# Optimization experiments

Hardware: AMD Instinct MI355X
Metric: run time of the kernel (lower is better)

Reference implementation:

```python
import jax, jax.numpy as jnp
import numpy as np

SQRT2 = 1.4142135623730951

def _gelu(x):
    return x * 0.5 * (1.0 + jax.lax.erf(x / SQRT2))

def _layer_norm(x, w, b, eps=1e-12):
    u = x.mean(-1, keepdims=True)
    s = ((x - u) ** 2).mean(-1, keepdims=True)
    return w * (x - u) / jnp.sqrt(s + eps) + b

def _rel_shift(x):
    # Transformer-XL relative shift: x is [b, n, q, p] -> shifted [b, n, q, p]
    b, n, q, p = x.shape
    x = jnp.concatenate([jnp.zeros((b, n, q, 1), x.dtype), x], axis=-1)
    x = x.reshape(b, n, p + 1, q)[:, :, 1:, :].reshape(b, n, q, p)
    return x

def setup_inputs() -> dict:
    key = jax.random.key(0)
    B, L, H, N = 4, 2048, 512, 8
    D = H // N
    ks = jax.random.split(key, 20)
    s = 0.02
    inp = {
        'x': jax.random.normal(ks[0], (B, L, H), jnp.float32),
        'pos_enc': jax.random.normal(ks[1], (L, H), jnp.float32),
        'Wq': jax.random.normal(ks[2], (N, H, D), jnp.float32) * s,
        'bq': jax.random.normal(ks[3], (N, D), jnp.float32) * s,
        'Wk': jax.random.normal(ks[4], (N, H, D), jnp.float32) * s,
        'bk': jax.random.normal(ks[5], (N, D), jnp.float32) * s,
        'Wv': jax.random.normal(ks[6], (N, H, D), jnp.float32) * s,
        'bv': jax.random.normal(ks[7], (N, D), jnp.float32) * s,
        'Wr': jax.random.normal(ks[8], (N, H, D), jnp.float32) * s,
        'br': jax.random.normal(ks[9], (N, D), jnp.float32) * s,
        'content_bias': jax.random.normal(ks[10], (N, D), jnp.float32) * s,
        'pos_bias': jax.random.normal(ks[11], (N, D), jnp.float32) * s,
        'Wc': jax.random.normal(ks[12], (H, H), jnp.float32) * s,
        'bc': jax.random.normal(ks[13], (H,), jnp.float32) * s,
        'W1': jax.random.normal(ks[14], (H, H), jnp.float32) * s,
        'b1': jax.random.normal(ks[15], (H,), jnp.float32) * s,
        'W2': jax.random.normal(ks[16], (H, H), jnp.float32) * s,
        'b2': jax.random.normal(ks[17], (H,), jnp.float32) * s,
        'ln_w': jnp.ones((H,), jnp.float32),
        'ln_b': jnp.zeros((H,), jnp.float32),
        # causal mask (True = masked out), as in subbatch_masks
        'mask': jnp.triu(jnp.ones((L, L), bool), k=1),
    }
    return inp

def reference(x, pos_enc, Wq, bq, Wk, bk, Wv, bv, Wr, br, content_bias, pos_bias,
              Wc, bc, W1, b1, W2, b2, ln_w, ln_b, mask):
    B, L, H = x.shape
    N, _, D = Wq.shape
    # per-head projections (LinearSplit)
    q = jnp.einsum('blh,nhd->bnld', x, Wq) + bq[None, :, None, :]
    k = jnp.einsum('blh,nhd->bnld', x, Wk) + bk[None, :, None, :]
    v = jnp.einsum('blh,nhd->bnld', x, Wv) + bv[None, :, None, :]
    r = jnp.einsum('ph,nhd->npd', pos_enc, Wr) + br[:, None, :]  # [n, L, d]
    qc = q + content_bias[None, :, None, :]
    qp = q + pos_bias[None, :, None, :]
    # content + relative-position biased scores (Transformer-XL)
    scores = jnp.einsum('bnid,bnjd->bnij', qc, k)
    scores = scores + _rel_shift(jnp.einsum('bnid,npd->bnip', qp, r))
    scores = scores / jnp.sqrt(jnp.asarray(D, scores.dtype))
    m = mask[None, None, :, :]
    scores = jnp.where(m, jnp.finfo(scores.dtype).min, scores)
    w = jax.nn.softmax(scores, axis=-1)
    w = jnp.where(m, 0.0, w)
    out = jnp.einsum('bnij,bnjd->bnid', w, v)
    out = out.transpose(0, 2, 1, 3).reshape(B, L, H)
    a = out @ Wc.T + bc
    a = _layer_norm(a + x, ln_w, ln_b)
    h = _gelu(a @ W1.T + b1) @ W2.T + b2
    return _layer_norm(a + h, ln_w, ln_b)
```

## Files before the change

kernel.cpp:

```cpp
#include <hip/hip_runtime.h>
#include <math.h>

#define HDIM 512
#define LSEQ 2048
#define NH 8
#define DH 64
#define NEGBIG (-3.0e38f)

#define MODE_QDUAL  0
#define MODE_KV     1
#define MODE_VT     2
#define MODE_RE     3
#define MODE_B16RES 4
#define MODE_GELU   5

typedef short bf16x8 __attribute__((ext_vector_type(8)));
typedef float f32x4 __attribute__((ext_vector_type(4)));

__device__ __forceinline__ unsigned short f2b(float f) {
  union { float f; unsigned u; } x; x.f = f;
  unsigned r = x.u + 0x7FFF + ((x.u >> 16) & 1);
  return (unsigned short)(r >> 16);
}
__device__ __forceinline__ float b2f(unsigned short u) {
  union { unsigned u; float f; } x; x.u = ((unsigned)u) << 16;
  return x.f;
}

__device__ __forceinline__ void gl_lds16(const void* g, void* l) {
  __builtin_amdgcn_global_load_lds(
      (const __attribute__((address_space(1))) void*)g,
      (__attribute__((address_space(3))) void*)l, 16, 0, 0);
}

__global__ __launch_bounds__(256) void conv_all(
    const float* __restrict__ x, const float* __restrict__ pos,
    const float* __restrict__ Wq, const float* __restrict__ Wk,
    const float* __restrict__ Wv, const float* __restrict__ Wr,
    const float* __restrict__ Wc, const float* __restrict__ W1,
    const float* __restrict__ W2,
    unsigned short* __restrict__ xb, unsigned short* __restrict__ posb,
    unsigned short* __restrict__ wT)
{
  const int t = threadIdx.x;
  const int z = blockIdx.z;
  if (z == 0) {
    int idx = blockIdx.x * 256 + t;
    float4 v = ((const float4*)x)[idx];
    ushort4 o; o.x = f2b(v.x); o.y = f2b(v.y); o.z = f2b(v.z); o.w = f2b(v.w);
    ((ushort4*)xb)[idx] = o;
  } else if (z == 1) {
    int idx = blockIdx.x * 256 + t;
    if (idx < 262144) {
      float4 v = ((const float4*)pos)[idx];
      ushort4 o; o.x = f2b(v.x); o.y = f2b(v.y); o.z = f2b(v.z); o.w = f2b(v.w);
      ((ushort4*)posb)[idx] = o;
    }
  } else {
    if (blockIdx.x >= 448) return;
    const int widx = blockIdx.x >> 6;
    const int tile = blockIdx.x & 63;
    const float* src = (widx == 0) ? Wq : (widx == 1) ? Wk : (widx == 2) ? Wv :
                       (widx == 3) ? Wr : (widx == 4) ? Wc : (widx == 5) ? W1 : W2;
    unsigned short* dst = wT + (size_t)widx * 262144;
    if (widx < 4) {
      __shared__ float td[64][65];
      const int h0 = (tile >> 3) * 64;
      const int n  = tile & 7;
      #pragma unroll
      for (int it = 0; it < 4; ++it) {
        int row = it * 16 + (t >> 4), dc = (t & 15) * 4;
        float4 v = *(const float4*)(src + (size_t)n * 32768 + (size_t)(h0 + row) * 64 + dc);
        td[row][dc] = v.x; td[row][dc + 1] = v.y; td[row][dc + 2] = v.z; td[row][dc + 3] = v.w;
      }
      __syncthreads();
      #pragma unroll
      for (int it = 0; it < 4; ++it) {
        int d = it * 16 + (t >> 4), h4 = (t & 15) * 4;
        ushort4 o;
        o.x = f2b(td[h4 + 0][d]); o.y = f2b(td[h4 + 1][d]);
        o.z = f2b(td[h4 + 2][d]); o.w = f2b(td[h4 + 3][d]);
        *(ushort4*)(dst + (size_t)(n * 64 + d) * 512 + h0 + h4) = o;
      }
    } else {
      #pragma unroll
      for (int i = 0; i < 4; ++i) {
        int f4 = tile * 1024 + i * 256 + t;
        float4 v = ((const float4*)src)[f4];
        ushort4 o; o.x = f2b(v.x); o.y = f2b(v.y); o.z = f2b(v.z); o.w = f2b(v.w);
        ((ushort4*)dst)[f4] = o;
      }
    }
  }
}

__device__ __forceinline__ void gemm_core(
    const unsigned short* __restrict__ A, const unsigned short* __restrict__ BT,
    const float* __restrict__ bias, const float* __restrict__ cb2,
    const float* __restrict__ pb2, const float* __restrict__ resf,
    const unsigned short* __restrict__ res16,
    void* __restrict__ C1v, unsigned short* __restrict__ C2, int mode,
    int bx, int by, char* SMEM)
{
  unsigned short* As = (unsigned short*)SMEM;
  unsigned short* Bs = (unsigned short*)(SMEM + 8192);

  const int t = threadIdx.x;
  const int w = t >> 6, lane = t & 63;
  const int l15 = lane & 15, quad = lane >> 4;
  const int r0 = by * 64;
  const int c0 = bx * 64;
  const int wm = (w >> 1) * 32, wc = (w & 1) * 32;

  f32x4 acc[2][2];
  #pragma unroll
  for (int sr = 0; sr < 2; ++sr)
    #pragma unroll
    for (int sc = 0; sc < 2; ++sc) acc[sr][sc] = (f32x4){0.f, 0.f, 0.f, 0.f};

  const int sub = lane >> 3;
  const int g   = (lane & 7) ^ sub;

  for (int k0 = 0; k0 < 512; k0 += 64) {
    __syncthreads();
    #pragma unroll
    for (int i = 0; i < 2; ++i) {
      int rowb = w * 16 + i * 8;
      gl_lds16(A  + (size_t)(r0 + rowb + sub) * 512 + k0 + g * 8, As + rowb * 64);
      gl_lds16(BT + (size_t)(c0 + rowb + sub) * 512 + k0 + g * 8, Bs + rowb * 64);
    }
    __syncthreads();

    #pragma unroll
    for (int kk = 0; kk < 2; ++kk) {
      bf16x8 af[2], bf[2];
      #pragma unroll
      for (int s = 0; s < 2; ++s) {
        int ar = wm + s * 16 + l15;
        af[s] = *(const bf16x8*)(As + ar * 64 + (((quad + 4 * kk) ^ (ar & 7)) << 3));
        int br = wc + s * 16 + l15;
        bf[s] = *(const bf16x8*)(Bs + br * 64 + (((quad + 4 * kk) ^ (br & 7)) << 3));
      }
      #pragma unroll
      for (int sr = 0; sr < 2; ++sr)
        #pragma unroll
        for (int sc = 0; sc < 2; ++sc)
          acc[sr][sc] = __builtin_amdgcn_mfma_f32_16x16x32_bf16(
              af[sr], bf[sc], acc[sr][sc], 0, 0, 0);
    }
  }

  __syncthreads();

  unsigned short* C1u = (unsigned short*)C1v;

  if (mode == MODE_VT) {
    unsigned short* LDb = (unsigned short*)SMEM;
    #pragma unroll
    for (int sc = 0; sc < 2; ++sc) {
      int cl = wc + sc * 16 + l15;
      float bia = bias[c0 + cl];
      #pragma unroll
      for (int sr = 0; sr < 2; ++sr)
        #pragma unroll
        for (int r = 0; r < 4; ++r) {
          int ml = wm + sr * 16 + quad * 4 + r;
          LDb[cl * 72 + ml] = f2b(acc[sr][sc][r] + bia);
        }
    }
    __syncthreads();
    int row = t >> 2;
    int c = c0 + row, n = c >> 6, d = c & 63;
    #pragma unroll
    for (int j = 0; j < 2; ++j) {
      int mcol = (t & 3) * 16 + j * 8;
      int4 val = *(const int4*)(LDb + row * 72 + mcol);
      int m = r0 + mcol, bb = m >> 11, l = m & 2047;
      *(int4*)(C1u + ((size_t)(bb * NH + n) * DH + d) * LSEQ + l) = val;
    }
  } else {
    unsigned short* LDb = (unsigned short*)SMEM;
    const int passes = (mode == MODE_QDUAL) ? 2 : 1;
    for (int p = 0; p < passes; ++p) {
      #pragma unroll
      for (int sc = 0; sc < 2; ++sc) {
        int cl = wc + sc * 16 + l15;
        int c = c0 + cl;
        float bia = bias[c];
        float ex = (mode == MODE_QDUAL) ? ((p == 0) ? cb2[c] : pb2[c]) : 0.f;
        #pragma unroll
        for (int sr = 0; sr < 2; ++sr)
          #pragma unroll
          for (int r = 0; r < 4; ++r) {
            int ml = wm + sr * 16 + quad * 4 + r;
            float v = acc[sr][sc][r] + bia;
            if (mode == MODE_QDUAL) v = (v + ex) * 0.125f;
            if (mode == MODE_GELU)
              v = 0.5f * v * (1.0f + erff(v * 0.70710678118654752f));
            LDb[ml * 72 + cl] = f2b(v);
          }
      }
      __syncthreads();
      int row = t >> 2;
      #pragma unroll
      for (int j = 0; j < 2; ++j) {
        int col = (t & 3) * 16 + j * 8;
        int4 val = *(const int4*)(LDb + row * 72 + col);
        unsigned short* dst;
        int c = c0 + col, n = c >> 6, d = c & 63;
        if (mode == MODE_RE) {
          int m = r0 + row;
          dst = C1u + ((size_t)n * LSEQ + (LSEQ - 1 - m)) * DH + d;
        } else if (mode == MODE_GELU) {
          dst = C1u + (size_t)(r0 + row) * 512 + c0 + col;
        } else if (mode == MODE_B16RES) {
          int m = r0 + row;
          size_t gofs = (size_t)m * 512 + c0 + col;
          unsigned short tmp[8];
          *(int4*)tmp = val;
          if (resf) {
            float4 ra = *(const float4*)(resf + gofs);
            float4 rb = *(const float4*)(resf + gofs + 4);
            tmp[0] = f2b(b2f(tmp[0]) + ra.x); tmp[1] = f2b(b2f(tmp[1]) + ra.y);
            tmp[2] = f2b(b2f(tmp[2]) + ra.z); tmp[3] = f2b(b2f(tmp[3]) + ra.w);
            tmp[4] = f2b(b2f(tmp[4]) + rb.x); tmp[5] = f2b(b2f(tmp[5]) + rb.y);
            tmp[6] = f2b(b2f(tmp[6]) + rb.z); tmp[7] = f2b(b2f(tmp[7]) + rb.w);
          } else {
            ushort4 sa = *(const ushort4*)(res16 + gofs);
            ushort4 sb = *(const ushort4*)(res16 + gofs + 4);
            tmp[0] = f2b(b2f(tmp[0]) + b2f(sa.x)); tmp[1] = f2b(b2f(tmp[1]) + b2f(sa.y));
            tmp[2] = f2b(b2f(tmp[2]) + b2f(sa.z)); tmp[3] = f2b(b2f(tmp[3]) + b2f(sa.w));
            tmp[4] = f2b(b2f(tmp[4]) + b2f(sb.x)); tmp[5] = f2b(b2f(tmp[5]) + b2f(sb.y));
            tmp[6] = f2b(b2f(tmp[6]) + b2f(sb.z)); tmp[7] = f2b(b2f(tmp[7]) + b2f(sb.w));
          }
          val = *(int4*)tmp;
          dst = C1u + gofs;
        } else {
          int m = r0 + row, bb = m >> 11, l = m & 2047;
          dst = ((p == 0) ? C1u : C2) + ((size_t)(bb * NH + n) * LSEQ + l) * DH + d;
        }
        *(int4*)dst = val;
      }
      if (p + 1 < passes) __syncthreads();
    }
  }
}

__global__ __launch_bounds__(256, 4) void gemm_mfma(
    const unsigned short* __restrict__ A, const unsigned short* __restrict__ BT,
    const float* __restrict__ bias, const float* __restrict__ resf,
    const unsigned short* __restrict__ res16,
    void* __restrict__ C1v, int mode)
{
  __shared__ __align__(16) char SMEM[16384];
  gemm_core(A, BT, bias, nullptr, nullptr, resf, res16, C1v, nullptr, mode,
            blockIdx.x, blockIdx.y, SMEM);
}

__global__ __launch_bounds__(256, 4) void qkv_fused(
    const unsigned short* __restrict__ xb, const unsigned short* __restrict__ posb,
    const unsigned short* __restrict__ WqT, const unsigned short* __restrict__ WkT,
    const unsigned short* __restrict__ WvT, const unsigned short* __restrict__ WrT,
    const float* __restrict__ bq, const float* __restrict__ bk,
    const float* __restrict__ bv, const float* __restrict__ br,
    const float* __restrict__ cbv, const float* __restrict__ pbv,
    unsigned short* __restrict__ qcb, unsigned short* __restrict__ qpb,
    unsigned short* __restrict__ kbb, unsigned short* __restrict__ vtb,
    unsigned short* __restrict__ rebb)
{
  __shared__ __align__(16) char SMEM[16384];
  const int z = blockIdx.z;
  if (z == 0) {
    gemm_core(xb, WqT, bq, cbv, pbv, nullptr, nullptr, qcb, qpb, MODE_QDUAL,
              blockIdx.x, blockIdx.y, SMEM);
  } else if (z == 1) {
    gemm_core(xb, WkT, bk, nullptr, nullptr, nullptr, nullptr, kbb, nullptr, MODE_KV,
              blockIdx.x, blockIdx.y, SMEM);
  } else if (z == 2) {
    gemm_core(xb, WvT, bv, nullptr, nullptr, nullptr, nullptr, vtb, nullptr, MODE_VT,
              blockIdx.x, blockIdx.y, SMEM);
  } else {
    if (blockIdx.y >= 32) return;
    gemm_core(posb, WrT, br, nullptr, nullptr, nullptr, nullptr, rebb, nullptr, MODE_RE,
              blockIdx.x, blockIdx.y, SMEM);
  }
}

#define PROW(i) ((i) * 72 + (((i) >> 2) << 3))

__global__ __launch_bounds__(256, 3) void attn_mfma(
    const unsigned short* __restrict__ qcb, const unsigned short* __restrict__ qpb,
    const unsigned short* __restrict__ kbb, const unsigned short* __restrict__ vtb,
    const unsigned short* __restrict__ rebb, unsigned short* __restrict__ outb)
{
  __shared__ __align__(16) unsigned short Ks[64 * 72];
  __shared__ __align__(16) unsigned short Vts[64 * 72];
  __shared__ __align__(16) unsigned short Res[128 * 72];
  __shared__ __align__(16) unsigned short TPb[4 * 16 * 84];

  const int t = threadIdx.x;
  const int bn = blockIdx.x;
  const int b = bn >> 3, n = bn & 7;
  const int ib = 31 - blockIdx.y;
  const int i0 = ib * 64;
  const int w = t >> 6;
  const int lane = t & 63;
  const int l15 = lane & 15, quad = lane >> 4;

  bf16x8 qcf[2], qpf[2];
  {
    size_t base = ((size_t)bn * LSEQ + i0 + 16 * w + l15) * DH + quad * 8;
    qcf[0] = *(const bf16x8*)(qcb + base);
    qcf[1] = *(const bf16x8*)(qcb + base + 32);
    qpf[0] = *(const bf16x8*)(qpb + base);
    qpf[1] = *(const bf16x8*)(qpb + base + 32);
  }

  f32x4 Of[4];
  #pragma unroll
  for (int s = 0; s < 4; ++s) Of[s] = (f32x4){0.f, 0.f, 0.f, 0.f};
  float lsum[4] = {0.f, 0.f, 0.f, 0.f};

  unsigned short* Tw = TPb + w * 1344;
  const int Ibase = i0 + 16 * w;
  const int nt = ib + 1;

  const int r2 = t >> 2, gl2 = t & 3;
  const int r1 = t >> 1, h1 = t & 1;

  for (int tt = 0; tt < nt; ++tt) {
    const int j0 = tt * 64;
    const int db = i0 - j0;

    const int4* skp = (const int4*)(kbb + ((size_t)bn * LSEQ + j0 + r2) * DH + gl2 * 16);
    int4 ka0 = skp[0], ka1 = skp[1];
    const int4* svp = (const int4*)(vtb + ((size_t)bn * DH + r2) * LSEQ + j0 + gl2 * 16);
    int4 va0 = svp[0], va1 = svp[1];
    int dist = db - 63 + r1;
    int4 ra[2][2];
    #pragma unroll
    for (int gi = 0; gi < 2; ++gi) {
      if (dist >= 0 && dist < LSEQ) {
        const int4* srp = (const int4*)(rebb + ((size_t)n * LSEQ + dist) * DH + (h1 * 2 + gi) * 16);
        ra[gi][0] = srp[0]; ra[gi][1] = srp[1];
      } else {
        int4 z = {0, 0, 0, 0};
        ra[gi][0] = z; ra[gi][1] = z;
      }
    }
    __syncthreads();
    {
      unsigned short* dk = Ks + r2 * 72 + ((gl2 ^ (r2 & 3)) * 16);
      *(int4*)(dk) = ka0; *(int4*)(dk + 8) = ka1;
      unsigned short* dv = Vts + r2 * 72 + ((gl2 ^ (r2 & 3)) * 16);
      *(int4*)(dv) = va0; *(int4*)(dv + 8) = va1;
      #pragma unroll
      for (int gi = 0; gi < 2; ++gi) {
        int gl = h1 * 2 + gi;
        unsigned short* dr = Res + r1 * 72 + ((gl ^ (r1 & 3)) * 16);
        *(int4*)(dr) = ra[gi][0]; *(int4*)(dr + 8) = ra[gi][1];
      }
    }
    __syncthreads();

    f32x4 Sf[4];
    #pragma unroll
    for (int s = 0; s < 4; ++s) {
      f32x4 acc = {0.f, 0.f, 0.f, 0.f};
      int row = 16 * s + l15;
      #pragma unroll
      for (int kk = 0; kk < 2; ++kk) {
        int g = (quad >> 1) + 2 * kk;
        bf16x8 bfr = *(const bf16x8*)(Ks + row * 72 + ((g ^ (row & 3)) * 16) + (quad & 1) * 8);
        acc = __builtin_amdgcn_mfma_f32_16x16x32_bf16(qcf[kk], bfr, acc, 0, 0, 0);
      }
      Sf[s] = acc;
    }
    #pragma unroll
    for (int s = 0; s < 5; ++s) {
      f32x4 acc = {0.f, 0.f, 0.f, 0.f};
      int row = 16 * w + 16 * s + l15;
      #pragma unroll
      for (int kk = 0; kk < 2; ++kk) {
        int g = (quad >> 1) + 2 * kk;
        bf16x8 bfr = *(const bf16x8*)(Res + row * 72 + ((g ^ (row & 3)) * 16) + (quad & 1) * 8);
        acc = __builtin_amdgcn_mfma_f32_16x16x32_bf16(qpf[kk], bfr, acc, 0, 0, 0);
      }
      #pragma unroll
      for (int r = 0; r < 4; ++r) {
        int i = quad * 4 + r;
        Tw[i * 84 + 16 * s + l15] = f2b(acc[r]);
      }
    }
    asm volatile("s_waitcnt lgkmcnt(0)" ::: "memory");

    float p_s[4][4];
    #pragma unroll
    for (int s = 0; s < 4; ++s)
      #pragma unroll
      for (int r = 0; r < 4; ++r) {
        int i = quad * 4 + r;
        float tval = b2f(Tw[i * 84 + 63 + i - 16 * s - l15]);
        float v = Sf[s][r] + tval;
        int j = j0 + 16 * s + l15;
        float p = (j <= Ibase + i) ? __expf(v) : 0.0f;
        p_s[s][r] = p;
        lsum[r] += p;
      }
    #pragma unroll
    for (int s = 0; s < 4; ++s)
      #pragma unroll
      for (int r = 0; r < 4; ++r) {
        int i = quad * 4 + r;
        Tw[PROW(i) + ((s ^ (i & 3)) * 16) + l15] = f2b(p_s[s][r]);
      }
    asm volatile("s_waitcnt lgkmcnt(0)" ::: "memory");

    #pragma unroll
    for (int kk = 0; kk < 2; ++kk) {
      int g = (quad >> 1) + 2 * kk;
      bf16x8 pa = *(const bf16x8*)(Tw + PROW(l15) + ((g ^ (l15 & 3)) * 16) + (quad & 1) * 8);
      #pragma unroll
      for (int s = 0; s < 4; ++s) {
        int d = 16 * s + l15;
        bf16x8 vb8 = *(const bf16x8*)(Vts + d * 72 + ((g ^ (d & 3)) * 16) + (quad & 1) * 8);
        Of[s] = __builtin_amdgcn_mfma_f32_16x16x32_bf16(pa, vb8, Of[s], 0, 0, 0);
      }
    }
  }

  #pragma unroll
  for (int r = 0; r < 4; ++r) {
    float rs = lsum[r];
    rs += __shfl_xor(rs, 1, 64);
    rs += __shfl_xor(rs, 2, 64);
    rs += __shfl_xor(rs, 4, 64);
    rs += __shfl_xor(rs, 8, 64);
    float linv = 1.0f / rs;
    int I = Ibase + quad * 4 + r;
    size_t base = ((size_t)b * LSEQ + I) * HDIM + n * DH;
    #pragma unroll
    for (int s = 0; s < 4; ++s)
      outb[base + 16 * s + l15] = f2b(Of[s][r] * linv);
  }
}

__global__ __launch_bounds__(256) void ln_b16(
    const unsigned short* __restrict__ xin, const float* __restrict__ w,
    const float* __restrict__ bb, float* __restrict__ outf,
    unsigned short* __restrict__ out16)
{
  const int t = threadIdx.x;
  const int lane = t & 63;
  const int row = blockIdx.x * 4 + (t >> 6);
  const size_t base = (size_t)row * 512 + lane * 8;

  unsigned short v16[8];
  *(int4*)v16 = *(const int4*)(xin + base);
  float v[8];
  float s = 0.f;
  #pragma unroll
  for (int i = 0; i < 8; ++i) { v[i] = b2f(v16[i]); s += v[i]; }
  #pragma unroll
  for (int off = 32; off >= 1; off >>= 1) s += __shfl_xor(s, off, 64);
  float mean = s * (1.0f / 512.0f);
  float s2 = 0.f;
  #pragma unroll
  for (int i = 0; i < 8; ++i) { float d = v[i] - mean; s2 += d * d; }
  #pragma unroll
  for (int off = 32; off >= 1; off >>= 1) s2 += __shfl_xor(s2, off, 64);
  float inv = 1.0f / sqrtf(s2 * (1.0f / 512.0f) + 1e-12f);

  float4 wa = *(const float4*)(w + lane * 8);
  float4 wb = *(const float4*)(w + lane * 8 + 4);
  float4 ba = *(const float4*)(bb + lane * 8);
  float4 bbv = *(const float4*)(bb + lane * 8 + 4);
  float o[8];
  o[0] = wa.x * (v[0] - mean) * inv + ba.x;
  o[1] = wa.y * (v[1] - mean) * inv + ba.y;
  o[2] = wa.z * (v[2] - mean) * inv + ba.z;
  o[3] = wa.w * (v[3] - mean) * inv + ba.w;
  o[4] = wb.x * (v[4] - mean) * inv + bbv.x;
  o[5] = wb.y * (v[5] - mean) * inv + bbv.y;
  o[6] = wb.z * (v[6] - mean) * inv + bbv.z;
  o[7] = wb.w * (v[7] - mean) * inv + bbv.w;
  if (outf) {
    float4 f0 = {o[0], o[1], o[2], o[3]}, f1 = {o[4], o[5], o[6], o[7]};
    *(float4*)(outf + base) = f0;
    *(float4*)(outf + base + 4) = f1;
  }
  if (out16) {
    unsigned short u[8];
    #pragma unroll
    for (int i = 0; i < 8; ++i) u[i] = f2b(o[i]);
    *(int4*)(out16 + base) = *(int4*)u;
  }
}

extern "C" void kernel_launch(void* const* d_in, const int* in_sizes, int n_in,
                              void* d_out, int out_size, void* d_ws, size_t ws_size,
                              hipStream_t stream)
{
  (void)in_sizes; (void)n_in; (void)out_size; (void)ws_size;
  const float* x   = (const float*)d_in[0];
  const float* pos = (const float*)d_in[1];
  const float* Wq  = (const float*)d_in[2];
  const float* bq  = (const float*)d_in[3];
  const float* Wk  = (const float*)d_in[4];
  const float* bk  = (const float*)d_in[5];
  const float* Wv  = (const float*)d_in[6];
  const float* bv  = (const float*)d_in[7];
  const float* Wr  = (const float*)d_in[8];
  const float* br  = (const float*)d_in[9];
  const float* cbv = (const float*)d_in[10];
  const float* pbv = (const float*)d_in[11];
  const float* Wc  = (const float*)d_in[12];
  const float* bc  = (const float*)d_in[13];
  const float* W1  = (const float*)d_in[14];
  const float* b1  = (const float*)d_in[15];
  const float* W2  = (const float*)d_in[16];
  const float* b2  = (const float*)d_in[17];
  const float* lnw = (const float*)d_in[18];
  const float* lnb = (const float*)d_in[19];
  char* ws = (char*)d_ws;
  float* outp = (float*)d_out;

  unsigned short* xb   = (unsigned short*)(ws);
  unsigned short* posb = (unsigned short*)(ws + 8388608);
  unsigned short* wT   = (unsigned short*)(ws + 10485760);
  unsigned short* qcb  = (unsigned short*)(ws + 14155776);
  unsigned short* qpb  = (unsigned short*)(ws + 22544384);
  unsigned short* kbb  = (unsigned short*)(ws + 30932992);
  unsigned short* vtb  = (unsigned short*)(ws + 39321600);
  unsigned short* rebb = (unsigned short*)(ws + 47710208);
  unsigned short* WqT = wT;
  unsigned short* WkT = wT + 262144;
  unsigned short* WvT = wT + 2 * 262144;
  unsigned short* WrT = wT + 3 * 262144;
  unsigned short* WcT = wT + 4 * 262144;
  unsigned short* W1T = wT + 5 * 262144;
  unsigned short* W2T = wT + 6 * 262144;
  unsigned short* attnb  = (unsigned short*)d_out;
  unsigned short* cpre16 = (unsigned short*)(ws + 14155776);
  unsigned short* ab16   = (unsigned short*)(ws);
  unsigned short* h1b    = (unsigned short*)(ws + 30932992);
  unsigned short* h2b16  = (unsigned short*)(ws + 22544384);

  dim3 blk(256);
  dim3 g8(8, 128);

  conv_all<<<dim3(4096, 1, 3), blk, 0, stream>>>(
      x, pos, Wq, Wk, Wv, Wr, Wc, W1, W2, xb, posb, wT);

  qkv_fused<<<dim3(8, 128, 4), blk, 0, stream>>>(
      xb, posb, WqT, WkT, WvT, WrT, bq, bk, bv, br, cbv, pbv,
      qcb, qpb, kbb, vtb, rebb);

  attn_mfma<<<dim3(32, 32), blk, 0, stream>>>(qcb, qpb, kbb, vtb, rebb, attnb);

  gemm_mfma<<<g8, blk, 0, stream>>>(attnb, WcT, bc, x, nullptr, cpre16, MODE_B16RES);
  ln_b16<<<2048, blk, 0, stream>>>(cpre16, lnw, lnb, nullptr, ab16);
  gemm_mfma<<<g8, blk, 0, stream>>>(ab16, W1T, b1, nullptr, nullptr, h1b, MODE_GELU);
  gemm_mfma<<<g8, blk, 0, stream>>>(h1b, W2T, b2, nullptr, ab16, h2b16, MODE_B16RES);
  ln_b16<<<2048, blk, 0, stream>>>(h2b16, lnw, lnb, outp, nullptr);
}
```

Measured before the change: 300.6 us.

## Fuse Q, K, V projections into one GEMM sharing the x tile

Replaces the per-projection z-slices of the QKV kernel with a single block that loads each x tile once into shared memory and runs MFMAs against the Wq, Wk and Wv tiles together, writing qc/qp, k and transposed v from separate epilogues. The R projection stays a separate z-slice. This cuts redundant A-tile global loads and the block count, but doubles shared memory to 32KB and triples accumulator registers per thread, which may reduce occupancy and leave fewer blocks to fill the GPU.

```diff
diff --git a/kernel.cpp b/kernel.cpp
--- a/kernel.cpp
+++ b/kernel.cpp
@@ -237,7 +237,7 @@
           dst = C1u + gofs;
         } else {
           int m = r0 + row, bb = m >> 11, l = m & 2047;
-          dst = ((p == 0) ? C1u : C2) + ((size_t)(bb * NH + n) * LSEQ + l) * DH + d;
+          dst = C1u + ((size_t)(bb * NH + n) * LSEQ + l) * DH + d;
         }
         *(int4*)dst = val;
       }
@@ -257,10 +257,9 @@
             blockIdx.x, blockIdx.y, SMEM);
 }
 
-__global__ __launch_bounds__(256, 4) void qkv_fused(
+__global__ __launch_bounds__(256, 4) void qkv3(
     const unsigned short* __restrict__ xb, const unsigned short* __restrict__ posb,
-    const unsigned short* __restrict__ WqT, const unsigned short* __restrict__ WkT,
-    const unsigned short* __restrict__ WvT, const unsigned short* __restrict__ WrT,
+    const unsigned short* __restrict__ wT,
     const float* __restrict__ bq, const float* __restrict__ bk,
     const float* __restrict__ bv, const float* __restrict__ br,
     const float* __restrict__ cbv, const float* __restrict__ pbv,
@@ -268,21 +267,162 @@
     unsigned short* __restrict__ kbb, unsigned short* __restrict__ vtb,
     unsigned short* __restrict__ rebb)
 {
-  __shared__ __align__(16) char SMEM[16384];
-  const int z = blockIdx.z;
-  if (z == 0) {
-    gemm_core(xb, WqT, bq, cbv, pbv, nullptr, nullptr, qcb, qpb, MODE_QDUAL,
-              blockIdx.x, blockIdx.y, SMEM);
-  } else if (z == 1) {
-    gemm_core(xb, WkT, bk, nullptr, nullptr, nullptr, nullptr, kbb, nullptr, MODE_KV,
-              blockIdx.x, blockIdx.y, SMEM);
-  } else if (z == 2) {
-    gemm_core(xb, WvT, bv, nullptr, nullptr, nullptr, nullptr, vtb, nullptr, MODE_VT,
-              blockIdx.x, blockIdx.y, SMEM);
-  } else {
-    if (blockIdx.y >= 32) return;
-    gemm_core(posb, WrT, br, nullptr, nullptr, nullptr, nullptr, rebb, nullptr, MODE_RE,
-              blockIdx.x, blockIdx.y, SMEM);
+  __shared__ __align__(16) char SMEM[32768];
+  if (blockIdx.z == 1) {
+    if (blockIdx.y < 32)
+      gemm_core(posb, wT + 3 * 262144, br, nullptr, nullptr, nullptr, nullptr,
+                rebb, nullptr, MODE_RE, blockIdx.x, blockIdx.y, SMEM);
+    return;
+  }
+
+  unsigned short* As  = (unsigned short*)SMEM;
+  unsigned short* Bqs = (unsigned short*)(SMEM + 8192);
+  unsigned short* Bks = (unsigned short*)(SMEM + 16384);
+  unsigned short* Bvs = (unsigned short*)(SMEM + 24576);
+  const unsigned short* WqT = wT;
+  const unsigned short* WkT = wT + 262144;
+  const unsigned short* WvT = wT + 2 * 262144;
+
+  const int t = threadIdx.x;
+  const int w = t >> 6, lane = t & 63;
+  const int l15 = lane & 15, quad = lane >> 4;
+  const int r0 = blockIdx.y * 64;
+  const int c0 = blockIdx.x * 64;
+  const int wm = (w >> 1) * 32, wc = (w & 1) * 32;
+
+  f32x4 accq[2][2], acck[2][2], accv[2][2];
+  #pragma unroll
+  for (int sr = 0; sr < 2; ++sr)
+    #pragma unroll
+    for (int sc = 0; sc < 2; ++sc) {
+      accq[sr][sc] = (f32x4){0.f, 0.f, 0.f, 0.f};
+      acck[sr][sc] = (f32x4){0.f, 0.f, 0.f, 0.f};
+      accv[sr][sc] = (f32x4){0.f, 0.f, 0.f, 0.f};
+    }
+
+  const int sub = lane >> 3;
+  const int g   = (lane & 7) ^ sub;
+
+  for (int k0 = 0; k0 < 512; k0 += 64) {
+    __syncthreads();
+    #pragma unroll
+    for (int i = 0; i < 2; ++i) {
+      int rowb = w * 16 + i * 8;
+      size_t asrc = (size_t)(r0 + rowb + sub) * 512 + k0 + g * 8;
+      size_t bsrc = (size_t)(c0 + rowb + sub) * 512 + k0 + g * 8;
+      gl_lds16(xb  + asrc, As  + rowb * 64);
+      gl_lds16(WqT + bsrc, Bqs + rowb * 64);
+      gl_lds16(WkT + bsrc, Bks + rowb * 64);
+      gl_lds16(WvT + bsrc, Bvs + rowb * 64);
+    }
+    __syncthreads();
+
+    #pragma unroll
+    for (int kk = 0; kk < 2; ++kk) {
+      bf16x8 af[2];
+      #pragma unroll
+      for (int s = 0; s < 2; ++s) {
+        int ar = wm + s * 16 + l15;
+        af[s] = *(const bf16x8*)(As + ar * 64 + (((quad + 4 * kk) ^ (ar & 7)) << 3));
+      }
+      #pragma unroll
+      for (int s = 0; s < 2; ++s) {
+        int br_ = wc + s * 16 + l15;
+        int off = br_ * 64 + (((quad + 4 * kk) ^ (br_ & 7)) << 3);
+        bf16x8 bq8 = *(const bf16x8*)(Bqs + off);
+        bf16x8 bk8 = *(const bf16x8*)(Bks + off);
+        bf16x8 bv8 = *(const bf16x8*)(Bvs + off);
+        #pragma unroll
+        for (int sr = 0; sr < 2; ++sr) {
+          accq[sr][s] = __builtin_amdgcn_mfma_f32_16x16x32_bf16(af[sr], bq8, accq[sr][s], 0, 0, 0);
+          acck[sr][s] = __builtin_amdgcn_mfma_f32_16x16x32_bf16(af[sr], bk8, acck[sr][s], 0, 0, 0);
+          accv[sr][s] = __builtin_amdgcn_mfma_f32_16x16x32_bf16(af[sr], bv8, accv[sr][s], 0, 0, 0);
+        }
+      }
+    }
+  }
+
+  unsigned short* LDb = (unsigned short*)SMEM;
+
+  #pragma unroll
+  for (int p = 0; p < 2; ++p) {
+    __syncthreads();
+    #pragma unroll
+    for (int sc = 0; sc < 2; ++sc) {
+      int cl = wc + sc * 16 + l15;
+      int c = c0 + cl;
+      float bia = bq[c] + ((p == 0) ? cbv[c] : pbv[c]);
+      #pragma unroll
+      for (int sr = 0; sr < 2; ++sr)
+        #pragma unroll
+        for (int r = 0; r < 4; ++r) {
+          int ml = wm + sr * 16 + quad * 4 + r;
+          LDb[ml * 72 + cl] = f2b((accq[sr][sc][r] + bia) * 0.125f);
+        }
+    }
+    __syncthreads();
+    int row = t >> 2;
+    unsigned short* C = (p == 0) ? qcb : qpb;
+    #pragma unroll
+    for (int j = 0; j < 2; ++j) {
+      int col = (t & 3) * 16 + j * 8;
+      int4 val = *(const int4*)(LDb + row * 72 + col);
+      int c = c0 + col, n = c >> 6, d = c & 63;
+      int m = r0 + row, bb = m >> 11, l = m & 2047;
+      *(int4*)(C + ((size_t)(bb * NH + n) * LSEQ + l) * DH + d) = val;
+    }
+  }
+
+  __syncthreads();
+  #pragma unroll
+  for (int sc = 0; sc < 2; ++sc) {
+    int cl = wc + sc * 16 + l15;
+    float bia = bk[c0 + cl];
+    #pragma unroll
+    for (int sr = 0; sr < 2; ++sr)
+      #pragma unroll
+      for (int r = 0; r < 4; ++r) {
+        int ml = wm + sr * 16 + quad * 4 + r;
+        LDb[ml * 72 + cl] = f2b(acck[sr][sc][r] + bia);
+      }
+  }
+  __syncthreads();
+  {
+    int row = t >> 2;
+    #pragma unroll
+    for (int j = 0; j < 2; ++j) {
+      int col = (t & 3) * 16 + j * 8;
+      int4 val = *(const int4*)(LDb + row * 72 + col);
+      int c = c0 + col, n = c >> 6, d = c & 63;
+      int m = r0 + row, bb = m >> 11, l = m & 2047;
+      *(int4*)(kbb + ((size_t)(bb * NH + n) * LSEQ + l) * DH + d) = val;
+    }
+  }
+
+  __syncthreads();
+  #pragma unroll
+  for (int sc = 0; sc < 2; ++sc) {
+    int cl = wc + sc * 16 + l15;
+    float bia = bv[c0 + cl];
+    #pragma unroll
+    for (int sr = 0; sr < 2; ++sr)
+      #pragma unroll
+      for (int r = 0; r < 4; ++r) {
+        int ml = wm + sr * 16 + quad * 4 + r;
+        LDb[cl * 72 + ml] = f2b(accv[sr][sc][r] + bia);
+      }
+  }
+  __syncthreads();
+  {
+    int row = t >> 2;
+    int c = c0 + row, n = c >> 6, d = c & 63;
+    #pragma unroll
+    for (int j = 0; j < 2; ++j) {
+      int mcol = (t & 3) * 16 + j * 8;
+      int4 val = *(const int4*)(LDb + row * 72 + mcol);
+      int m = r0 + mcol, bb = m >> 11, l = m & 2047;
+      *(int4*)(vtb + ((size_t)(bb * NH + n) * DH + d) * LSEQ + l) = val;
+    }
   }
 }
 
@@ -533,10 +673,6 @@
   unsigned short* kbb  = (unsigned short*)(ws + 30932992);
   unsigned short* vtb  = (unsigned short*)(ws + 39321600);
   unsigned short* rebb = (unsigned short*)(ws + 47710208);
-  unsigned short* WqT = wT;
-  unsigned short* WkT = wT + 262144;
-  unsigned short* WvT = wT + 2 * 262144;
-  unsigned short* WrT = wT + 3 * 262144;
   unsigned short* WcT = wT + 4 * 262144;
   unsigned short* W1T = wT + 5 * 262144;
   unsigned short* W2T = wT + 6 * 262144;
@@ -552,9 +688,8 @@
   conv_all<<<dim3(4096, 1, 3), blk, 0, stream>>>(
       x, pos, Wq, Wk, Wv, Wr, Wc, W1, W2, xb, posb, wT);
 
-  qkv_fused<<<dim3(8, 128, 4), blk, 0, stream>>>(
-      xb, posb, WqT, WkT, WvT, WrT, bq, bk, bv, br, cbv, pbv,
-      qcb, qpb, kbb, vtb, rebb);
+  qkv3<<<dim3(8, 128, 2), blk, 0, stream>>>(
+      xb, posb, wT, bq, bk, bv, br, cbv, pbv, qcb, qpb, kbb, vtb, rebb);
 
   attn_mfma<<<dim3(32, 32), blk, 0, stream>>>(qcb, qpb, kbb, vtb, rebb, attnb);
 
```

Result: no change. 296.7 us (-1.3%).
